# Performance work log

Hardware: AMD Instinct MI355X
Metric: run time of the kernel (lower is better)

The kernel has to match this reference:

```python
import jax, jax.numpy as jnp
import numpy as np

B, S, D_IN, D_ATT = 8, 2048, 512, 512
D_ROT = D_ATT // 2  # RotaryEmbedding(dim=attention_dim//2): only first half of features rotated


def _rotary(x):
    # x: [B, S, D_ATT]; rotate first D_ROT dims with interleaved-pair rotation (lucidrains style)
    seq = x.shape[1]
    inv_freq = 1.0 / (10000.0 ** (jnp.arange(0, D_ROT, 2, dtype=jnp.float32) / D_ROT))  # [D_ROT/2]
    freqs = jnp.arange(seq, dtype=jnp.float32)[:, None] * inv_freq[None, :]             # [S, D_ROT/2]
    freqs = jnp.repeat(freqs, 2, axis=-1)                                               # [S, D_ROT]
    cos, sin = jnp.cos(freqs), jnp.sin(freqs)
    xr = x[..., :D_ROT]
    x1, x2 = xr[..., 0::2], xr[..., 1::2]
    rot = jnp.stack((-x2, x1), axis=-1).reshape(xr.shape)  # rotate_half, interleaved pairs
    return jnp.concatenate([xr * cos + rot * sin, x[..., D_ROT:]], axis=-1)


def setup_inputs() -> dict:
    key = jax.random.key(0)
    ks = jax.random.split(key, 10)
    s = 1.0 / np.sqrt(D_IN)
    return {
        "query": jax.random.normal(ks[0], (B, S, D_IN), dtype=jnp.float32),
        "key": jax.random.normal(ks[1], (B, S, D_IN), dtype=jnp.float32),
        "value": jax.random.normal(ks[2], (B, S, D_IN), dtype=jnp.float32),
        "mask": jax.random.randint(ks[3], (B, S, S), 0, 2, dtype=jnp.int32),
        "Wq": jax.random.uniform(ks[4], (D_IN, D_ATT), jnp.float32, -s, s),
        "bq": jnp.zeros((D_ATT,), jnp.float32),
        "Wk": jax.random.uniform(ks[5], (D_IN, D_ATT), jnp.float32, -s, s),
        "bk": jnp.zeros((D_ATT,), jnp.float32),
        "Wv": jax.random.uniform(ks[6], (D_IN, D_ATT), jnp.float32, -s, s),
        "bv": jnp.zeros((D_ATT,), jnp.float32),
    }


def reference(query, key, value, mask, Wq, bq, Wk, bk, Wv, bv):
    q = query @ Wq + bq
    k = key @ Wk + bk
    v = value @ Wv + bv
    q = _rotary(q)
    k = _rotary(k)
    scores = jnp.einsum("bqd,bkd->bqk", q, k) / jnp.float32(np.sqrt(D_ATT))
    # faithful to source: masked positions get -1e-9 (note: source likely meant -1e9)
    scores = jnp.where(mask == 0, jnp.float32(-1e-9), scores)
    weights = jax.nn.softmax(scores, axis=-1)
    context = jnp.einsum("bqk,bkd->bqd", weights, v)
    return context, weights
```

## Files before the change

### kernel.cpp

```cpp
#include <hip/hip_runtime.h>
#include <hip/hip_bf16.h>
#include <hip/hip_fp16.h>

#define B_   8
#define S_   2048
#define DIN  512
#define DATT 512
#define DROT 256

typedef __attribute__((ext_vector_type(4))) float f32x4;
typedef __attribute__((ext_vector_type(8))) short bf16x8;
typedef __attribute__((ext_vector_type(8))) unsigned short u16x8;

__device__ __forceinline__ short f2bf(float f) {
    __hip_bfloat16 h = __float2bfloat16(f);
    return *reinterpret_cast<short*>(&h);
}
__device__ __forceinline__ unsigned short f2h(float f) {
    __half h = __float2half(f);
    return *reinterpret_cast<unsigned short*>(&h);
}
__device__ __forceinline__ float h2f(unsigned short u) {
    __half h = *reinterpret_cast<__half*>(&u);
    return __half2float(h);
}

__global__ __launch_bounds__(256) void k_prep(
    float* __restrict__ cosT, float* __restrict__ sinT,
    const float* __restrict__ Wq, const float* __restrict__ Wk,
    const float* __restrict__ Wv,
    short* __restrict__ WtQ, short* __restrict__ WtK, short* __restrict__ WtV)
{
    __shared__ float tile[64 * 68];
    int bid = blockIdx.x;
    int t = threadIdx.x;
    if (bid < 1024) {
        int idx = bid * 256 + t;
        int s = idx >> 7;
        int i = idx & 127;
        float e    = (float)(2 * i) / (float)DROT;
        float invf = 1.0f / powf(10000.0f, e);
        float f    = (float)s * invf;
        float c = cosf(f), sn = sinf(f);
        cosT[s * 256 + 2 * i]     = c;
        cosT[s * 256 + 2 * i + 1] = c;
        sinT[s * 256 + 2 * i]     = sn;
        sinT[s * 256 + 2 * i + 1] = sn;
        return;
    }
    int wi = bid - 1024;
    int mz = wi >> 6;
    int xi = wi & 63;
    const float* W; short* Wt;
    if (mz == 0)      { W = Wq; Wt = WtQ; }
    else if (mz == 1) { W = Wk; Wt = WtK; }
    else              { W = Wv; Wt = WtV; }
    int kt = xi & 7, nt = xi >> 3;
    int k0 = kt * 64, n0 = nt * 64;
    #pragma unroll
    for (int i = 0; i < 4; ++i) {
        int slot = t + 256 * i;
        int row = slot >> 4;
        int c4  = (slot & 15) * 4;
        float4 v = *(const float4*)&W[(size_t)(k0 + row) * DATT + n0 + c4];
        *(float4*)&tile[row * 68 + c4] = v;
    }
    __syncthreads();
    int nr = t >> 2, kq = (t & 3) * 16;
    bf16x8 o0, o1;
    #pragma unroll
    for (int j = 0; j < 8; ++j) o0[j] = f2bf(tile[(kq + j) * 68 + nr]);
    #pragma unroll
    for (int j = 0; j < 8; ++j) o1[j] = f2bf(tile[(kq + 8 + j) * 68 + nr]);
    *(bf16x8*)&Wt[(size_t)(n0 + nr) * DIN + k0 + kq]     = o0;
    *(bf16x8*)&Wt[(size_t)(n0 + nr) * DIN + k0 + kq + 8] = o1;
}

__global__ __launch_bounds__(256) void k_proj3(
    const float* __restrict__ Xq, const float* __restrict__ Xk,
    const float* __restrict__ Xv, const short* __restrict__ Wt0,
    const float* __restrict__ bq, const float* __restrict__ bk,
    const float* __restrict__ bv,
    short* __restrict__ Qb, short* __restrict__ Kb, short* __restrict__ Vb,
    const float* __restrict__ cosT, const float* __restrict__ sinT)
{
    int fid = blockIdx.x + 4 * (blockIdx.y + 128 * blockIdx.z);
    fid = (fid & 7) * 192 + (fid >> 3);
    int bx = fid & 3;
    int rem = fid >> 2;
    int by = rem & 127;
    int z  = rem >> 7;

    const float* X    = (z == 0) ? Xq : (z == 1) ? Xk : Xv;
    const float* bias = (z == 0) ? bq : (z == 1) ? bk : bv;
    short*       Out  = (z == 0) ? Qb : (z == 1) ? Kb : Vb;
    const short* Wt   = Wt0 + (size_t)z * DATT * DIN;
    int doRot = (z < 2);

    __shared__ __align__(16) float smem[8704];
    short* As = (short*)smem;
    short* Bs = (short*)(smem + 4608);
    float* Ct = smem;
    int t = threadIdx.x;
    int l = t & 63, w = t >> 6;
    int wr = (w >> 1) * 64, wc = (w & 1) * 64;
    int fr = l & 15, fk8 = (l >> 4) * 8;
    int xr = (fr & 7) << 3;
    int rowBase = by * 128;
    int nBase   = bx * 128;

    f32x4 acc[4][4] = {};
    int trA = t >> 4, tcA = (t & 15) * 4;
    int srow = w * 8 + (l >> 3);
    int skolsw = (((l & 7) ^ (l >> 3)) * 8);

    for (int k0 = 0; k0 < DIN; k0 += 64) {
        #pragma unroll
        for (int it = 0; it < 4; ++it) {
            int r = it * 32 + srow;
            __builtin_amdgcn_global_load_lds(
                (const __attribute__((address_space(1))) void*)
                    &Wt[(size_t)(nBase + r) * DIN + k0 + skolsw],
                (__attribute__((address_space(3))) void*)
                    &Bs[(it * 32 + w * 8) * 64],
                16, 0, 0);
        }
        #pragma unroll
        for (int ii = 0; ii < 8; ++ii) {
            int r = ii * 16 + trA;
            float4 v = *(const float4*)&X[(size_t)(rowBase + r) * DIN + k0 + tcA];
            short4 s4 = make_short4(f2bf(v.x), f2bf(v.y), f2bf(v.z), f2bf(v.w));
            *(short4*)&As[r * 72 + tcA] = s4;
        }
        __syncthreads();
        #pragma unroll
        for (int kk = 0; kk < 64; kk += 32) {
            bf16x8 af[4], bfr[4];
            #pragma unroll
            for (int m = 0; m < 4; ++m)
                af[m] = *(const bf16x8*)&As[(wr + m * 16 + fr) * 72 + kk + fk8];
            #pragma unroll
            for (int n = 0; n < 4; ++n)
                bfr[n] = *(const bf16x8*)&Bs[(wc + n * 16 + fr) * 64 + ((kk + fk8) ^ xr)];
            #pragma unroll
            for (int m = 0; m < 4; ++m)
                #pragma unroll
                for (int n = 0; n < 4; ++n)
                    acc[m][n] = __builtin_amdgcn_mfma_f32_16x16x32_bf16(af[m], bfr[n], acc[m][n], 0, 0, 0);
        }
        __syncthreads();
    }

    for (int ch = 0; ch < 4; ++ch) {
        if ((w & 1) == (ch >> 1)) {
            int nb = (ch & 1) * 2;
            #pragma unroll
            for (int n2 = 0; n2 < 2; ++n2)
                #pragma unroll
                for (int m = 0; m < 4; ++m)
                    #pragma unroll
                    for (int q = 0; q < 4; ++q)
                        Ct[(wr + m * 16 + (l >> 4) * 4 + q) * 34 + n2 * 16 + fr]
                            = acc[m][nb + n2][q];
        }
        __syncthreads();
        {
            int r = t >> 1, seg = (t & 1) * 16;
            int rg = rowBase + r;
            int cg = nBase + ch * 32 + seg;
            float vv[16];
            #pragma unroll
            for (int u = 0; u < 4; ++u)
                *(float4*)&vv[4 * u] = *(float4*)&Ct[r * 34 + seg + 4 * u];
            #pragma unroll
            for (int u = 0; u < 4; ++u) {
                float4 bb = *(const float4*)&bias[cg + 4 * u];
                vv[4 * u + 0] += bb.x; vv[4 * u + 1] += bb.y;
                vv[4 * u + 2] += bb.z; vv[4 * u + 3] += bb.w;
            }
            if (doRot && cg < DROT) {
                int s = rg & (S_ - 1);
                float cs[16], sn[16];
                #pragma unroll
                for (int u = 0; u < 4; ++u) {
                    *(float4*)&cs[4 * u] = *(const float4*)&cosT[s * 256 + cg + 4 * u];
                    *(float4*)&sn[4 * u] = *(const float4*)&sinT[s * 256 + cg + 4 * u];
                }
                #pragma unroll
                for (int j = 0; j < 16; j += 2) {
                    float x1 = vv[j], x2 = vv[j + 1];
                    vv[j]     = x1 * cs[j]     - x2 * sn[j];
                    vv[j + 1] = x2 * cs[j + 1] + x1 * sn[j + 1];
                }
            }
            bf16x8 o0, o1;
            #pragma unroll
            for (int j = 0; j < 8; ++j) { o0[j] = f2bf(vv[j]); o1[j] = f2bf(vv[8 + j]); }
            *(bf16x8*)&Out[(size_t)rg * DATT + cg]     = o0;
            *(bf16x8*)&Out[(size_t)rg * DATT + cg + 8] = o1;
        }
        __syncthreads();
    }
}

__global__ __launch_bounds__(256) void k_vt(
    const short* __restrict__ Vb, short* __restrict__ Vt)
{
    int b = blockIdx.z;
    int d0 = blockIdx.x * 64;
    int r0 = blockIdx.y * 64;
    const short* Vp = Vb + (size_t)b * S_ * DATT;
    short* Tp = Vt + (size_t)b * DATT * S_;
    __shared__ short tile[64 * 66];
    int t = threadIdx.x;
    #pragma unroll
    for (int i = 0; i < 2; ++i) {
        int slot = t + 256 * i;
        int row = slot >> 3;
        int c8  = (slot & 7) * 8;
        bf16x8 v = *(const bf16x8*)&Vp[(size_t)(r0 + row) * DATT + d0 + c8];
        #pragma unroll
        for (int j = 0; j < 8; ++j) tile[row * 66 + c8 + j] = v[j];
    }
    __syncthreads();
    int dr = t >> 2, rq = (t & 3) * 16;
    bf16x8 o0, o1;
    #pragma unroll
    for (int j = 0; j < 8; ++j) o0[j] = tile[(rq + j) * 66 + dr];
    #pragma unroll
    for (int j = 0; j < 8; ++j) o1[j] = tile[(rq + 8 + j) * 66 + dr];
    *(bf16x8*)&Tp[(size_t)(d0 + dr) * S_ + r0 + rq]     = o0;
    *(bf16x8*)&Tp[(size_t)(d0 + dr) * S_ + r0 + rq + 8] = o1;
}

__global__ __launch_bounds__(256) void k_scores_h(
    const short* __restrict__ Qb, const short* __restrict__ Kb,
    unsigned short* __restrict__ Sraw)
{
    int fid = blockIdx.x + 16 * (blockIdx.y + 16 * blockIdx.z);
    fid = (fid & 7) * 256 + (fid >> 3);
    int bxs = fid & 15;
    int rem = fid >> 4;
    int bys = rem & 15;
    int b   = rem >> 4;

    __shared__ __align__(16) float smem[8192];
    short* As = (short*)smem;
    short* Bs = (short*)(smem + 4096);
    float* Ct = smem;
    int t = threadIdx.x;
    int l = t & 63, w = t >> 6;
    int wr = (w >> 1) * 64, wc = (w & 1) * 64;
    int fr = l & 15, fk8 = (l >> 4) * 8;
    int xr = (fr & 7) << 3;
    int iBase = bys * 128;
    int jBase = bxs * 128;
    const short* Qp = Qb + (size_t)b * S_ * DATT;
    const short* Kp = Kb + (size_t)b * S_ * DATT;

    f32x4 acc[4][4] = {};
    int srow = w * 8 + (l >> 3);
    int skolsw = (((l & 7) ^ (l >> 3)) * 8);

    for (int k0 = 0; k0 < DATT; k0 += 64) {
        #pragma unroll
        for (int it = 0; it < 4; ++it) {
            int r = it * 32 + srow;
            __builtin_amdgcn_global_load_lds(
                (const __attribute__((address_space(1))) void*)
                    &Qp[(size_t)(iBase + r) * DATT + k0 + skolsw],
                (__attribute__((address_space(3))) void*)
                    &As[(it * 32 + w * 8) * 64],
                16, 0, 0);
            __builtin_amdgcn_global_load_lds(
                (const __attribute__((address_space(1))) void*)
                    &Kp[(size_t)(jBase + r) * DATT + k0 + skolsw],
                (__attribute__((address_space(3))) void*)
                    &Bs[(it * 32 + w * 8) * 64],
                16, 0, 0);
        }
        __syncthreads();
        #pragma unroll
        for (int kk = 0; kk < 64; kk += 32) {
            bf16x8 af[4], bfr[4];
            #pragma unroll
            for (int m = 0; m < 4; ++m)
                af[m] = *(const bf16x8*)&As[(wr + m * 16 + fr) * 64 + ((kk + fk8) ^ xr)];
            #pragma unroll
            for (int n = 0; n < 4; ++n)
                bfr[n] = *(const bf16x8*)&Bs[(wc + n * 16 + fr) * 64 + ((kk + fk8) ^ xr)];
            #pragma unroll
            for (int m = 0; m < 4; ++m)
                #pragma unroll
                for (int n = 0; n < 4; ++n)
                    acc[m][n] = __builtin_amdgcn_mfma_f32_16x16x32_bf16(af[m], bfr[n], acc[m][n], 0, 0, 0);
        }
        __syncthreads();
    }

    const float scale = 0.04419417382415922f;
    for (int ch = 0; ch < 4; ++ch) {
        if ((w & 1) == (ch >> 1)) {
            int nb = (ch & 1) * 2;
            #pragma unroll
            for (int n2 = 0; n2 < 2; ++n2)
                #pragma unroll
                for (int m = 0; m < 4; ++m)
                    #pragma unroll
                    for (int q = 0; q < 4; ++q)
                        Ct[(wr + m * 16 + (l >> 4) * 4 + q) * 34 + n2 * 16 + fr]
                            = acc[m][nb + n2][q] * scale;
        }
        __syncthreads();
        {
            int r = t >> 1, seg = (t & 1) * 16;
            size_t base = ((size_t)b * S_ + iBase + r) * S_ + jBase + ch * 32 + seg;
            float vv[16];
            #pragma unroll
            for (int u = 0; u < 4; ++u)
                *(float4*)&vv[4 * u] = *(float4*)&Ct[r * 34 + seg + 4 * u];
            u16x8 h0, h1;
            #pragma unroll
            for (int j = 0; j < 8; ++j) { h0[j] = f2h(vv[j]); h1[j] = f2h(vv[8 + j]); }
            *(u16x8*)&Sraw[base]     = h0;
            *(u16x8*)&Sraw[base + 8] = h1;
        }
        __syncthreads();
    }
}

__global__ __launch_bounds__(256) void k_softmax_h(
    unsigned short* __restrict__ SrawPb, const int* __restrict__ mask,
    float* __restrict__ wts)
{
    size_t row = blockIdx.x;
    unsigned short* sp = SrawPb + row * S_;
    const int* mp = mask + row * S_;
    float* wp = wts + row * S_;
    int t = threadIdx.x, l = t & 63, w = t >> 6;

    u16x8 raw = *(const u16x8*)&sp[8 * t];
    int4 m0 = *(const int4*)&mp[8 * t];
    int4 m1 = *(const int4*)&mp[8 * t + 4];
    float v[8];
    v[0] = (m0.x == 0) ? -1e-9f : h2f(raw[0]);
    v[1] = (m0.y == 0) ? -1e-9f : h2f(raw[1]);
    v[2] = (m0.z == 0) ? -1e-9f : h2f(raw[2]);
    v[3] = (m0.w == 0) ? -1e-9f : h2f(raw[3]);
    v[4] = (m1.x == 0) ? -1e-9f : h2f(raw[4]);
    v[5] = (m1.y == 0) ? -1e-9f : h2f(raw[5]);
    v[6] = (m1.z == 0) ? -1e-9f : h2f(raw[6]);
    v[7] = (m1.w == 0) ? -1e-9f : h2f(raw[7]);

    float mx = v[0];
    #pragma unroll
    for (int j = 1; j < 8; ++j) mx = fmaxf(mx, v[j]);
    for (int off = 32; off; off >>= 1) mx = fmaxf(mx, __shfl_xor(mx, off));
    __shared__ float red[8];
    if (l == 0) red[w] = mx;
    __syncthreads();
    mx = fmaxf(fmaxf(red[0], red[1]), fmaxf(red[2], red[3]));
    float sum = 0.f;
    #pragma unroll
    for (int j = 0; j < 8; ++j) { v[j] = expf(v[j] - mx); sum += v[j]; }
    for (int off = 32; off; off >>= 1) sum += __shfl_xor(sum, off);
    if (l == 0) red[4 + w] = sum;
    __syncthreads();
    sum = red[4] + red[5] + red[6] + red[7];
    float inv = 1.0f / sum;
    #pragma unroll
    for (int j = 0; j < 8; ++j) v[j] *= inv;

    *(float4*)&wp[8 * t]     = make_float4(v[0], v[1], v[2], v[3]);
    *(float4*)&wp[8 * t + 4] = make_float4(v[4], v[5], v[6], v[7]);
    bf16x8 pb8;
    #pragma unroll
    for (int j = 0; j < 8; ++j) pb8[j] = f2bf(v[j]);
    *(bf16x8*)&sp[8 * t] = pb8;
}

__global__ __launch_bounds__(256) void k_ctx_bf16(
    const short* __restrict__ Pb, const short* __restrict__ Vt,
    float* __restrict__ ctx)
{
    int fid = blockIdx.x + 4 * (blockIdx.y + 16 * blockIdx.z);
    fid = (fid & 7) * 64 + (fid >> 3);
    int bxs = fid & 3;
    int rem = fid >> 2;
    int bys = rem & 15;
    int b   = rem >> 4;

    __shared__ __align__(16) float smem[8192];
    short* As = (short*)smem;
    short* Bs = (short*)(smem + 4096);
    float* Ct = smem;
    int t = threadIdx.x;
    int l = t & 63, w = t >> 6;
    int wr = (w >> 1) * 64, wc = (w & 1) * 64;
    int fr = l & 15, fk8 = (l >> 4) * 8;
    int xr = (fr & 7) << 3;
    int iBase = bys * 128;
    int nBase = bxs * 128;
    const short* Ap = Pb + (size_t)b * S_ * S_;
    const short* Bp = Vt + (size_t)b * DATT * S_;

    f32x4 acc[4][4] = {};
    int srow = w * 8 + (l >> 3);
    int skolsw = (((l & 7) ^ (l >> 3)) * 8);

    for (int k0 = 0; k0 < S_; k0 += 64) {
        #pragma unroll
        for (int it = 0; it < 4; ++it) {
            int r = it * 32 + srow;
            __builtin_amdgcn_global_load_lds(
                (const __attribute__((address_space(1))) void*)
                    &Ap[(size_t)(iBase + r) * S_ + k0 + skolsw],
                (__attribute__((address_space(3))) void*)
                    &As[(it * 32 + w * 8) * 64],
                16, 0, 0);
            __builtin_amdgcn_global_load_lds(
                (const __attribute__((address_space(1))) void*)
                    &Bp[(size_t)(nBase + r) * S_ + k0 + skolsw],
                (__attribute__((address_space(3))) void*)
                    &Bs[(it * 32 + w * 8) * 64],
                16, 0, 0);
        }
        __syncthreads();
        #pragma unroll
        for (int kk = 0; kk < 64; kk += 32) {
            bf16x8 af[4], bfr[4];
            #pragma unroll
            for (int m = 0; m < 4; ++m)
                af[m] = *(const bf16x8*)&As[(wr + m * 16 + fr) * 64 + ((kk + fk8) ^ xr)];
            #pragma unroll
            for (int n = 0; n < 4; ++n)
                bfr[n] = *(const bf16x8*)&Bs[(wc + n * 16 + fr) * 64 + ((kk + fk8) ^ xr)];
            #pragma unroll
            for (int m = 0; m < 4; ++m)
                #pragma unroll
                for (int n = 0; n < 4; ++n)
                    acc[m][n] = __builtin_amdgcn_mfma_f32_16x16x32_bf16(af[m], bfr[n], acc[m][n], 0, 0, 0);
        }
        __syncthreads();
    }

    for (int ch = 0; ch < 4; ++ch) {
        if ((w & 1) == (ch >> 1)) {
            int nb = (ch & 1) * 2;
            #pragma unroll
            for (int n2 = 0; n2 < 2; ++n2)
                #pragma unroll
                for (int m = 0; m < 4; ++m)
                    #pragma unroll
                    for (int q = 0; q < 4; ++q)
                        Ct[(wr + m * 16 + (l >> 4) * 4 + q) * 34 + n2 * 16 + fr]
                            = acc[m][nb + n2][q];
        }
        __syncthreads();
        {
            int r = t >> 1, seg = (t & 1) * 16;
            int gi = iBase + r;
            size_t base = ((size_t)b * S_ + gi) * DATT + nBase + ch * 32 + seg;
            #pragma unroll
            for (int u = 0; u < 4; ++u) {
                float4 vv = *(float4*)&Ct[r * 34 + seg + 4 * u];
                *(float4*)&ctx[base + 4 * u] = vv;
            }
        }
        __syncthreads();
    }
}

__global__ __launch_bounds__(256) void k_scores_f32(
    const short* __restrict__ Qb, const short* __restrict__ Kb,
    const int* __restrict__ mask, float* __restrict__ wOut)
{
    __shared__ __align__(16) float smem[4352];
    short* As = (short*)smem;
    short* Bs = (short*)(smem + 2048);
    float* Ct = smem;
    int t = threadIdx.x;
    int l = t & 63, w = t >> 6;
    int wr = (w >> 1) * 64, wc = (w & 1) * 64;
    int fr = l & 15, fk = (l >> 4) * 8;
    int b = blockIdx.z;
    int iBase = blockIdx.y * 128;
    int jBase = blockIdx.x * 128;
    const short* Qp = Qb + (size_t)b * S_ * DATT;
    const short* Kp = Kb + (size_t)b * S_ * DATT;

    f32x4 acc[4][4] = {};
    int srow = w * 16 + (l >> 2);
    int skol = (l & 3) * 8;

    for (int k0 = 0; k0 < DATT; k0 += 32) {
        #pragma unroll
        for (int it = 0; it < 2; ++it) {
            int r = it * 64 + srow;
            __builtin_amdgcn_global_load_lds(
                (const __attribute__((address_space(1))) void*)
                    &Qp[(size_t)(iBase + r) * DATT + k0 + skol],
                (__attribute__((address_space(3))) void*)
                    &As[(it * 64 + w * 16) * 32],
                16, 0, 0);
            __builtin_amdgcn_global_load_lds(
                (const __attribute__((address_space(1))) void*)
                    &Kp[(size_t)(jBase + r) * DATT + k0 + skol],
                (__attribute__((address_space(3))) void*)
                    &Bs[(it * 64 + w * 16) * 32],
                16, 0, 0);
        }
        __syncthreads();
        bf16x8 af[4], bfr[4];
        #pragma unroll
        for (int m = 0; m < 4; ++m)
            af[m] = *(const bf16x8*)&As[(wr + m * 16 + fr) * 32 + fk];
        #pragma unroll
        for (int n = 0; n < 4; ++n)
            bfr[n] = *(const bf16x8*)&Bs[(wc + n * 16 + fr) * 32 + fk];
        #pragma unroll
        for (int m = 0; m < 4; ++m)
            #pragma unroll
            for (int n = 0; n < 4; ++n)
                acc[m][n] = __builtin_amdgcn_mfma_f32_16x16x32_bf16(af[m], bfr[n], acc[m][n], 0, 0, 0);
        __syncthreads();
    }

    const float scale = 0.04419417382415922f;
    for (int ch = 0; ch < 4; ++ch) {
        if ((w & 1) == (ch >> 1)) {
            int nb = (ch & 1) * 2;
            #pragma unroll
            for (int n2 = 0; n2 < 2; ++n2)
                #pragma unroll
                for (int m = 0; m < 4; ++m)
                    #pragma unroll
                    for (int q = 0; q < 4; ++q)
                        Ct[(wr + m * 16 + (l >> 4) * 4 + q) * 34 + n2 * 16 + fr]
                            = acc[m][nb + n2][q] * scale;
        }
        __syncthreads();
        {
            int r = t >> 1, seg = (t & 1) * 16;
            size_t base = ((size_t)b * S_ + iBase + r) * S_ + jBase + ch * 32 + seg;
            #pragma unroll
            for (int u = 0; u < 4; ++u) {
                float4 vv = *(float4*)&Ct[r * 34 + seg + 4 * u];
                int4  mm = *(const int4*)&mask[base + 4 * u];
                vv.x = (mm.x == 0) ? -1e-9f : vv.x;
                vv.y = (mm.y == 0) ? -1e-9f : vv.y;
                vv.z = (mm.z == 0) ? -1e-9f : vv.z;
                vv.w = (mm.w == 0) ? -1e-9f : vv.w;
                *(float4*)&wOut[base + 4 * u] = vv;
            }
        }
        __syncthreads();
    }
}

__global__ __launch_bounds__(256) void k_softmax_f32(float* __restrict__ wts) {
    size_t row = blockIdx.x;
    float* p = wts + row * S_;
    int t = threadIdx.x, l = t & 63, w = t >> 6;
    float v[8];
    *(float4*)&v[0] = ((const float4*)p)[t];
    *(float4*)&v[4] = ((const float4*)p)[t + 256];
    float mx = v[0];
    #pragma unroll
    for (int j = 1; j < 8; ++j) mx = fmaxf(mx, v[j]);
    for (int off = 32; off; off >>= 1) mx = fmaxf(mx, __shfl_xor(mx, off));
    __shared__ float red[8];
    if (l == 0) red[w] = mx;
    __syncthreads();
    mx = fmaxf(fmaxf(red[0], red[1]), fmaxf(red[2], red[3]));
    float sum = 0.f;
    #pragma unroll
    for (int j = 0; j < 8; ++j) { v[j] = expf(v[j] - mx); sum += v[j]; }
    for (int off = 32; off; off >>= 1) sum += __shfl_xor(sum, off);
    if (l == 0) red[4 + w] = sum;
    __syncthreads();
    sum = red[4] + red[5] + red[6] + red[7];
    float inv = 1.0f / sum;
    #pragma unroll
    for (int j = 0; j < 8; ++j) v[j] *= inv;
    ((float4*)p)[t]       = *(float4*)&v[0];
    ((float4*)p)[t + 256] = *(float4*)&v[4];
}

__global__ __launch_bounds__(256) void k_ctx_f32(
    const float* __restrict__ wts, const short* __restrict__ Vt,
    float* __restrict__ ctx)
{
    __shared__ short As[128 * 40];
    __shared__ short Bs[128 * 32];
    int t = threadIdx.x;
    int l = t & 63, w = t >> 6;
    int wr = (w >> 1) * 64, wc = (w & 1) * 64;
    int fr = l & 15, fk = (l >> 4) * 8;
    int b = blockIdx.z;
    int iBase = blockIdx.y * 128;
    int nBase = blockIdx.x * 128;
    const float* Wp = wts + (size_t)b * S_ * S_;
    const short* Bp = Vt + (size_t)b * DATT * S_;

    f32x4 acc[4][4] = {};
    int trA = t >> 3, tcA = (t & 7) * 4;
    int srow = w * 16 + (l >> 2), skol = (l & 3) * 8;

    for (int k0 = 0; k0 < S_; k0 += 32) {
        #pragma unroll
        for (int it = 0; it < 2; ++it) {
            int r = it * 64 + srow;
            __builtin_amdgcn_global_load_lds(
                (const __attribute__((address_space(1))) void*)
                    &Bp[(size_t)(nBase + r) * S_ + k0 + skol],
                (__attribute__((address_space(3))) void*)
                    &Bs[(it * 64 + w * 16) * 32],
                16, 0, 0);
        }
        #pragma unroll
        for (int ii = 0; ii < 4; ++ii) {
            int r = trA + 32 * ii;
            float4 v = *(const float4*)&Wp[(size_t)(iBase + r) * S_ + k0 + tcA];
            short4 s4 = make_short4(f2bf(v.x), f2bf(v.y), f2bf(v.z), f2bf(v.w));
            *(short4*)&As[r * 40 + tcA] = s4;
        }
        __syncthreads();
        bf16x8 af[4], bfr[4];
        #pragma unroll
        for (int m = 0; m < 4; ++m)
            af[m] = *(const bf16x8*)&As[(wr + m * 16 + fr) * 40 + fk];
        #pragma unroll
        for (int n = 0; n < 4; ++n)
            bfr[n] = *(const bf16x8*)&Bs[(wc + n * 16 + fr) * 32 + fk];
        #pragma unroll
        for (int m = 0; m < 4; ++m)
            #pragma unroll
            for (int n = 0; n < 4; ++n)
                acc[m][n] = __builtin_amdgcn_mfma_f32_16x16x32_bf16(af[m], bfr[n], acc[m][n], 0, 0, 0);
        __syncthreads();
    }

    for (int m = 0; m < 4; ++m) {
        for (int q = 0; q < 4; ++q) {
            int i = iBase + wr + m * 16 + (l >> 4) * 4 + q;
            for (int n = 0; n < 4; ++n) {
                int d = nBase + wc + n * 16 + fr;
                ctx[((size_t)b * S_ + i) * DATT + d] = acc[m][n][q];
            }
        }
    }
}

extern "C" void kernel_launch(void* const* d_in, const int* in_sizes, int n_in,
                              void* d_out, int out_size, void* d_ws, size_t ws_size,
                              hipStream_t stream) {
    const float* query = (const float*)d_in[0];
    const float* key   = (const float*)d_in[1];
    const float* value = (const float*)d_in[2];
    const int*   mask  = (const int*)d_in[3];
    const float* Wq = (const float*)d_in[4];
    const float* bq = (const float*)d_in[5];
    const float* Wk = (const float*)d_in[6];
    const float* bk = (const float*)d_in[7];
    const float* Wv = (const float*)d_in[8];
    const float* bv = (const float*)d_in[9];

    float* ctx = (float*)d_out;
    float* wts = ctx + (size_t)B_ * S_ * DATT;

    char* ws = (char*)d_ws;
    const size_t SZ_QKV = (size_t)B_ * S_ * DATT * 2;
    const size_t SZ_WT  = (size_t)DATT * DIN * 2;
    const size_t SZ_TAB = (size_t)S_ * 256 * 4;
    short* Qb   = (short*)(ws);
    short* Kb   = (short*)(ws + SZ_QKV);
    short* Vt   = (short*)(ws + 2 * SZ_QKV);
    short* WtQ  = (short*)(ws + 3 * SZ_QKV);
    float* cosT = (float*)(ws + 3 * SZ_QKV + 3 * SZ_WT);
    float* sinT = (float*)(ws + 3 * SZ_QKV + 3 * SZ_WT + SZ_TAB);
    char*  big  = ws + 3 * SZ_QKV + 3 * SZ_WT + 2 * SZ_TAB;
    short* Vb   = (short*)big;
    unsigned short* Sraw = (unsigned short*)big;
    const size_t needA = 3 * SZ_QKV + 3 * SZ_WT + 2 * SZ_TAB
                       + (size_t)B_ * S_ * S_ * 2;
    int useH = ws_size >= needA ? 1 : 0;

    short* WtK = WtQ + (size_t)DATT * DIN;
    short* WtV = WtK + (size_t)DATT * DIN;

    k_prep<<<dim3(1216), 256, 0, stream>>>(cosT, sinT, Wq, Wk, Wv, WtQ, WtK, WtV);
    k_proj3<<<dim3(4, 128, 3), 256, 0, stream>>>(query, key, value, WtQ,
                                                 bq, bk, bv, Qb, Kb, Vb,
                                                 cosT, sinT);
    k_vt<<<dim3(8, 32, 8), 256, 0, stream>>>(Vb, Vt);
    if (useH) {
        k_scores_h<<<dim3(16, 16, 8), 256, 0, stream>>>(Qb, Kb, Sraw);
        k_softmax_h<<<dim3(B_ * S_), 256, 0, stream>>>(Sraw, mask, wts);
        k_ctx_bf16<<<dim3(4, 16, 8), 256, 0, stream>>>((short*)Sraw, Vt, ctx);
    } else {
        k_scores_f32<<<dim3(16, 16, 8), 256, 0, stream>>>(Qb, Kb, mask, wts);
        k_softmax_f32<<<dim3(B_ * S_), 256, 0, stream>>>(wts);
        k_ctx_f32<<<dim3(4, 16, 8), 256, 0, stream>>>(wts, Vt, ctx);
    }
}
```

Measured before the change: 519.7 us.

## Double-buffer LDS tiles in projection, scores and context GEMM kernels

Converts the three bf16 MFMA GEMM main loops (QKV projection, QK^T scores, P·V context) to double-buffered LDS. The next K-tile's global-to-LDS loads are issued before the current tile's MFMAs, which removes one barrier per iteration and lets memory latency overlap compute. In the projection kernel the fp32 X tile is prefetched into registers and converted and stored to the alternate buffer after the MFMAs. LDS use per block doubles to about 64-68 KB, which may reduce how many blocks fit per CU.

```diff
diff --git a/kernel.cpp b/kernel.cpp
--- a/kernel.cpp
+++ b/kernel.cpp
@@ -97,10 +97,10 @@
     const short* Wt   = Wt0 + (size_t)z * DATT * DIN;
     int doRot = (z < 2);
 
-    __shared__ __align__(16) float smem[8704];
-    short* As = (short*)smem;
-    short* Bs = (short*)(smem + 4608);
-    float* Ct = smem;
+    __shared__ __align__(16) float smem[17408];
+    short* Asb = (short*)smem;
+    short* Bsb = (short*)(smem + 9216);
+    float* Ct  = smem;
     int t = threadIdx.x;
     int l = t & 63, w = t >> 6;
     int wr = (w >> 1) * 64, wc = (w & 1) * 64;
@@ -114,39 +114,74 @@
     int srow = w * 8 + (l >> 3);
     int skolsw = (((l & 7) ^ (l >> 3)) * 8);
 
-    for (int k0 = 0; k0 < DIN; k0 += 64) {
-        #pragma unroll
-        for (int it = 0; it < 4; ++it) {
-            int r = it * 32 + srow;
-            __builtin_amdgcn_global_load_lds(
-                (const __attribute__((address_space(1))) void*)
-                    &Wt[(size_t)(nBase + r) * DIN + k0 + skolsw],
-                (__attribute__((address_space(3))) void*)
-                    &Bs[(it * 32 + w * 8) * 64],
-                16, 0, 0);
-        }
-        #pragma unroll
-        for (int ii = 0; ii < 8; ++ii) {
-            int r = ii * 16 + trA;
-            float4 v = *(const float4*)&X[(size_t)(rowBase + r) * DIN + k0 + tcA];
-            short4 s4 = make_short4(f2bf(v.x), f2bf(v.y), f2bf(v.z), f2bf(v.w));
-            *(short4*)&As[r * 72 + tcA] = s4;
-        }
-        __syncthreads();
-        #pragma unroll
-        for (int kk = 0; kk < 64; kk += 32) {
-            bf16x8 af[4], bfr[4];
-            #pragma unroll
-            for (int m = 0; m < 4; ++m)
-                af[m] = *(const bf16x8*)&As[(wr + m * 16 + fr) * 72 + kk + fk8];
-            #pragma unroll
-            for (int n = 0; n < 4; ++n)
-                bfr[n] = *(const bf16x8*)&Bs[(wc + n * 16 + fr) * 64 + ((kk + fk8) ^ xr)];
-            #pragma unroll
-            for (int m = 0; m < 4; ++m)
+    float4 xv[8];
+    #pragma unroll
+    for (int ii = 0; ii < 8; ++ii)
+        xv[ii] = *(const float4*)&X[(size_t)(rowBase + ii * 16 + trA) * DIN + tcA];
+    #pragma unroll
+    for (int it = 0; it < 4; ++it) {
+        int r = it * 32 + srow;
+        __builtin_amdgcn_global_load_lds(
+            (const __attribute__((address_space(1))) void*)
+                &Wt[(size_t)(nBase + r) * DIN + skolsw],
+            (__attribute__((address_space(3))) void*)
+                &Bsb[(it * 32 + w * 8) * 64],
+            16, 0, 0);
+    }
+    #pragma unroll
+    for (int ii = 0; ii < 8; ++ii) {
+        short4 s4 = make_short4(f2bf(xv[ii].x), f2bf(xv[ii].y),
+                                f2bf(xv[ii].z), f2bf(xv[ii].w));
+        *(short4*)&Asb[(ii * 16 + trA) * 72 + tcA] = s4;
+    }
+    __syncthreads();
+
+    for (int kt = 0; kt < 8; ++kt) {
+        int cur = kt & 1;
+        if (kt < 7) {
+            int k1 = (kt + 1) * 64;
+            #pragma unroll
+            for (int ii = 0; ii < 8; ++ii)
+                xv[ii] = *(const float4*)&X[(size_t)(rowBase + ii * 16 + trA) * DIN + k1 + tcA];
+            short* Bd = Bsb + (cur ^ 1) * 8192;
+            #pragma unroll
+            for (int it = 0; it < 4; ++it) {
+                int r = it * 32 + srow;
+                __builtin_amdgcn_global_load_lds(
+                    (const __attribute__((address_space(1))) void*)
+                        &Wt[(size_t)(nBase + r) * DIN + k1 + skolsw],
+                    (__attribute__((address_space(3))) void*)
+                        &Bd[(it * 32 + w * 8) * 64],
+                    16, 0, 0);
+            }
+        }
+        {
+            short* Ac = Asb + cur * 9216;
+            short* Bc = Bsb + cur * 8192;
+            #pragma unroll
+            for (int kk = 0; kk < 64; kk += 32) {
+                bf16x8 af[4], bfr[4];
+                #pragma unroll
+                for (int m = 0; m < 4; ++m)
+                    af[m] = *(const bf16x8*)&Ac[(wr + m * 16 + fr) * 72 + kk + fk8];
                 #pragma unroll
                 for (int n = 0; n < 4; ++n)
-                    acc[m][n] = __builtin_amdgcn_mfma_f32_16x16x32_bf16(af[m], bfr[n], acc[m][n], 0, 0, 0);
+                    bfr[n] = *(const bf16x8*)&Bc[(wc + n * 16 + fr) * 64 + ((kk + fk8) ^ xr)];
+                #pragma unroll
+                for (int m = 0; m < 4; ++m)
+                    #pragma unroll
+                    for (int n = 0; n < 4; ++n)
+                        acc[m][n] = __builtin_amdgcn_mfma_f32_16x16x32_bf16(af[m], bfr[n], acc[m][n], 0, 0, 0);
+            }
+        }
+        if (kt < 7) {
+            short* Ad = Asb + (cur ^ 1) * 9216;
+            #pragma unroll
+            for (int ii = 0; ii < 8; ++ii) {
+                short4 s4 = make_short4(f2bf(xv[ii].x), f2bf(xv[ii].y),
+                                        f2bf(xv[ii].z), f2bf(xv[ii].w));
+                *(short4*)&Ad[(ii * 16 + trA) * 72 + tcA] = s4;
+            }
         }
         __syncthreads();
     }
@@ -244,10 +279,10 @@
     int bys = rem & 15;
     int b   = rem >> 4;
 
-    __shared__ __align__(16) float smem[8192];
-    short* As = (short*)smem;
-    short* Bs = (short*)(smem + 4096);
-    float* Ct = smem;
+    __shared__ __align__(16) float smem[16384];
+    short* Asb = (short*)smem;
+    short* Bsb = (short*)(smem + 8192);
+    float* Ct  = smem;
     int t = threadIdx.x;
     int l = t & 63, w = t >> 6;
     int wr = (w >> 1) * 64, wc = (w & 1) * 64;
@@ -262,33 +297,58 @@
     int srow = w * 8 + (l >> 3);
     int skolsw = (((l & 7) ^ (l >> 3)) * 8);
 
-    for (int k0 = 0; k0 < DATT; k0 += 64) {
-        #pragma unroll
-        for (int it = 0; it < 4; ++it) {
-            int r = it * 32 + srow;
-            __builtin_amdgcn_global_load_lds(
-                (const __attribute__((address_space(1))) void*)
-                    &Qp[(size_t)(iBase + r) * DATT + k0 + skolsw],
-                (__attribute__((address_space(3))) void*)
-                    &As[(it * 32 + w * 8) * 64],
-                16, 0, 0);
-            __builtin_amdgcn_global_load_lds(
-                (const __attribute__((address_space(1))) void*)
-                    &Kp[(size_t)(jBase + r) * DATT + k0 + skolsw],
-                (__attribute__((address_space(3))) void*)
-                    &Bs[(it * 32 + w * 8) * 64],
-                16, 0, 0);
-        }
-        __syncthreads();
+    #pragma unroll
+    for (int it = 0; it < 4; ++it) {
+        int r = it * 32 + srow;
+        __builtin_amdgcn_global_load_lds(
+            (const __attribute__((address_space(1))) void*)
+                &Qp[(size_t)(iBase + r) * DATT + skolsw],
+            (__attribute__((address_space(3))) void*)
+                &Asb[(it * 32 + w * 8) * 64],
+            16, 0, 0);
+        __builtin_amdgcn_global_load_lds(
+            (const __attribute__((address_space(1))) void*)
+                &Kp[(size_t)(jBase + r) * DATT + skolsw],
+            (__attribute__((address_space(3))) void*)
+                &Bsb[(it * 32 + w * 8) * 64],
+            16, 0, 0);
+    }
+    __syncthreads();
+
+    for (int kt = 0; kt < 8; ++kt) {
+        int cur = kt & 1;
+        if (kt < 7) {
+            int k1 = (kt + 1) * 64;
+            short* Ad = Asb + (cur ^ 1) * 8192;
+            short* Bd = Bsb + (cur ^ 1) * 8192;
+            #pragma unroll
+            for (int it = 0; it < 4; ++it) {
+                int r = it * 32 + srow;
+                __builtin_amdgcn_global_load_lds(
+                    (const __attribute__((address_space(1))) void*)
+                        &Qp[(size_t)(iBase + r) * DATT + k1 + skolsw],
+                    (__attribute__((address_space(3))) void*)
+                        &Ad[(it * 32 + w * 8) * 64],
+                    16, 0, 0);
+                __builtin_amdgcn_global_load_lds(
+                    (const __attribute__((address_space(1))) void*)
+                        &Kp[(size_t)(jBase + r) * DATT + k1 + skolsw],
+                    (__attribute__((address_space(3))) void*)
+                        &Bd[(it * 32 + w * 8) * 64],
+                    16, 0, 0);
+            }
+        }
+        short* Ac = Asb + cur * 8192;
+        short* Bc = Bsb + cur * 8192;
         #pragma unroll
         for (int kk = 0; kk < 64; kk += 32) {
             bf16x8 af[4], bfr[4];
             #pragma unroll
             for (int m = 0; m < 4; ++m)
-                af[m] = *(const bf16x8*)&As[(wr + m * 16 + fr) * 64 + ((kk + fk8) ^ xr)];
+                af[m] = *(const bf16x8*)&Ac[(wr + m * 16 + fr) * 64 + ((kk + fk8) ^ xr)];
             #pragma unroll
             for (int n = 0; n < 4; ++n)
-                bfr[n] = *(const bf16x8*)&Bs[(wc + n * 16 + fr) * 64 + ((kk + fk8) ^ xr)];
+                bfr[n] = *(const bf16x8*)&Bc[(wc + n * 16 + fr) * 64 + ((kk + fk8) ^ xr)];
             #pragma unroll
             for (int m = 0; m < 4; ++m)
                 #pragma unroll
@@ -390,10 +450,10 @@
     int bys = rem & 15;
     int b   = rem >> 4;
 
-    __shared__ __align__(16) float smem[8192];
-    short* As = (short*)smem;
-    short* Bs = (short*)(smem + 4096);
-    float* Ct = smem;
+    __shared__ __align__(16) float smem[16384];
+    short* Asb = (short*)smem;
+    short* Bsb = (short*)(smem + 8192);
+    float* Ct  = smem;
     int t = threadIdx.x;
     int l = t & 63, w = t >> 6;
     int wr = (w >> 1) * 64, wc = (w & 1) * 64;
@@ -408,33 +468,58 @@
     int srow = w * 8 + (l >> 3);
     int skolsw = (((l & 7) ^ (l >> 3)) * 8);
 
-    for (int k0 = 0; k0 < S_; k0 += 64) {
-        #pragma unroll
-        for (int it = 0; it < 4; ++it) {
-            int r = it * 32 + srow;
-            __builtin_amdgcn_global_load_lds(
-                (const __attribute__((address_space(1))) void*)
-                    &Ap[(size_t)(iBase + r) * S_ + k0 + skolsw],
-                (__attribute__((address_space(3))) void*)
-                    &As[(it * 32 + w * 8) * 64],
-                16, 0, 0);
-            __builtin_amdgcn_global_load_lds(
-                (const __attribute__((address_space(1))) void*)
-                    &Bp[(size_t)(nBase + r) * S_ + k0 + skolsw],
-                (__attribute__((address_space(3))) void*)
-                    &Bs[(it * 32 + w * 8) * 64],
-                16, 0, 0);
-        }
-        __syncthreads();
+    #pragma unroll
+    for (int it = 0; it < 4; ++it) {
+        int r = it * 32 + srow;
+        __builtin_amdgcn_global_load_lds(
+            (const __attribute__((address_space(1))) void*)
+                &Ap[(size_t)(iBase + r) * S_ + skolsw],
+            (__attribute__((address_space(3))) void*)
+                &Asb[(it * 32 + w * 8) * 64],
+            16, 0, 0);
+        __builtin_amdgcn_global_load_lds(
+            (const __attribute__((address_space(1))) void*)
+                &Bp[(size_t)(nBase + r) * S_ + skolsw],
+            (__attribute__((address_space(3))) void*)
+                &Bsb[(it * 32 + w * 8) * 64],
+            16, 0, 0);
+    }
+    __syncthreads();
+
+    for (int kt = 0; kt < 32; ++kt) {
+        int cur = kt & 1;
+        if (kt < 31) {
+            int k1 = (kt + 1) * 64;
+            short* Ad = Asb + (cur ^ 1) * 8192;
+            short* Bd = Bsb + (cur ^ 1) * 8192;
+            #pragma unroll
+            for (int it = 0; it < 4; ++it) {
+                int r = it * 32 + srow;
+                __builtin_amdgcn_global_load_lds(
+                    (const __attribute__((address_space(1))) void*)
+                        &Ap[(size_t)(iBase + r) * S_ + k1 + skolsw],
+                    (__attribute__((address_space(3))) void*)
+                        &Ad[(it * 32 + w * 8) * 64],
+                    16, 0, 0);
+                __builtin_amdgcn_global_load_lds(
+                    (const __attribute__((address_space(1))) void*)
+                        &Bp[(size_t)(nBase + r) * S_ + k1 + skolsw],
+                    (__attribute__((address_space(3))) void*)
+                        &Bd[(it * 32 + w * 8) * 64],
+                    16, 0, 0);
+            }
+        }
+        short* Ac = Asb + cur * 8192;
+        short* Bc = Bsb + cur * 8192;
         #pragma unroll
         for (int kk = 0; kk < 64; kk += 32) {
             bf16x8 af[4], bfr[4];
             #pragma unroll
             for (int m = 0; m < 4; ++m)
-                af[m] = *(const bf16x8*)&As[(wr + m * 16 + fr) * 64 + ((kk + fk8) ^ xr)];
+                af[m] = *(const bf16x8*)&Ac[(wr + m * 16 + fr) * 64 + ((kk + fk8) ^ xr)];
             #pragma unroll
             for (int n = 0; n < 4; ++n)
-                bfr[n] = *(const bf16x8*)&Bs[(wc + n * 16 + fr) * 64 + ((kk + fk8) ^ xr)];
+                bfr[n] = *(const bf16x8*)&Bc[(wc + n * 16 + fr) * 64 + ((kk + fk8) ^ xr)];
             #pragma unroll
             for (int m = 0; m < 4; ++m)
                 #pragma unroll
```

Result: faster. 504.0 us (-3.0%).
